# Optimization experiments

Hardware: AMD Instinct MI355X
Metric: run time of the kernel (lower is better)

The kernel has to match this reference:

```python
import jax, jax.numpy as jnp
import numpy as np

B, S, HID = 2, 2048, 2304
NH, NKV, HD = 8, 4, 256
GROUPS = NH // NKV
SCALE = 256 ** -0.5          # query_pre_attn_scalar ** -0.5
SOFTCAP = 50.0               # attn_logit_softcapping
ROPE_THETA = 10000.0


def setup_inputs() -> dict:
    key = jax.random.key(0)
    ks = jax.random.split(key, 5)
    return {
        "hidden_states": jax.random.normal(ks[0], (B, S, HID), dtype=jnp.float32),
        "wq": jax.random.normal(ks[1], (HID, NH * HD), dtype=jnp.float32) * 0.02,
        "wk": jax.random.normal(ks[2], (HID, NKV * HD), dtype=jnp.float32) * 0.02,
        "wv": jax.random.normal(ks[3], (HID, NKV * HD), dtype=jnp.float32) * 0.02,
        "wo": jax.random.normal(ks[4], (NH * HD, HID), dtype=jnp.float32) * 0.02,
    }


def _rope_cos_sin(seq_len, dim, dtype):
    inv_freq = 1.0 / (ROPE_THETA ** (jnp.arange(0, dim, 2, dtype=jnp.float32) / dim))
    pos = jnp.arange(seq_len, dtype=jnp.float32)
    freqs = pos[:, None] * inv_freq[None, :]            # [S, HD/2]
    emb = jnp.concatenate([freqs, freqs], axis=-1)      # [S, HD]
    return jnp.cos(emb).astype(dtype), jnp.sin(emb).astype(dtype)


def _rotate_half(x):
    x1, x2 = jnp.split(x, 2, axis=-1)
    return jnp.concatenate([-x2, x1], axis=-1)


def reference(hidden_states, wq, wk, wv, wo):
    b, s, _ = hidden_states.shape
    # projections -> [B, H, S, D]
    q = (hidden_states @ wq).reshape(b, s, NH, HD).transpose(0, 2, 1, 3)
    k = (hidden_states @ wk).reshape(b, s, NKV, HD).transpose(0, 2, 1, 3)
    v = (hidden_states @ wv).reshape(b, s, NKV, HD).transpose(0, 2, 1, 3)

    cos, sin = _rope_cos_sin(s, HD, q.dtype)            # [S, HD]
    q = q * cos + _rotate_half(q) * sin
    k = k * cos + _rotate_half(k) * sin

    # GQA repeat_kv
    k = jnp.repeat(k, GROUPS, axis=1)                   # [B, NH, S, D]
    v = jnp.repeat(v, GROUPS, axis=1)

    scores = jnp.einsum("bhqd,bhkd->bhqk", q, k) * SCALE
    # tanh logit softcapping
    scores = SOFTCAP * jnp.tanh(scores / SOFTCAP)
    # causal additive mask
    neg = jnp.finfo(scores.dtype).min
    causal = jnp.tril(jnp.ones((s, s), dtype=bool))
    scores = jnp.where(causal[None, None], scores, neg)

    probs = jax.nn.softmax(scores, axis=-1).astype(q.dtype)
    attn = jnp.einsum("bhqk,bhkd->bhqd", probs, v)      # [B, NH, S, D]
    attn = attn.transpose(0, 2, 1, 3).reshape(b, s, NH * HD)
    return attn @ wo
```

## Files before the change

kernel.cpp:

```cpp
#include <hip/hip_runtime.h>
#include <hip/hip_bf16.h>

typedef __attribute__((ext_vector_type(8))) short short8;
typedef __attribute__((ext_vector_type(4))) float f32x4;
typedef __attribute__((ext_vector_type(4))) unsigned short ushort4_;
typedef __attribute__((ext_vector_type(2))) unsigned long ulong2_;

__device__ __forceinline__ unsigned short f2bf(float f) {
  unsigned u = __builtin_bit_cast(unsigned, f);
  u += 0x7fff + ((u >> 16) & 1);
  return (unsigned short)(u >> 16);
}

__device__ __forceinline__ void gload16(const unsigned short* g, unsigned short* l) {
  __builtin_amdgcn_global_load_lds((const __attribute__((address_space(1))) unsigned int*)g,
                                   (__attribute__((address_space(3))) unsigned int*)l, 16, 0, 0);
}

__global__ void sincos_kernel(float2* __restrict__ table) {
  int idx = blockIdx.x * 256 + threadIdx.x;
  int s = idx >> 7, i = idx & 127;
  float inv = exp2f(-(float)i * (13.287712379549449f / 128.0f));
  float ang = (float)s * inv;
  table[idx] = make_float2(cosf(ang), sinf(ang));
}

__global__ void convert_x_kernel(const float* __restrict__ in, unsigned short* __restrict__ out, int n4) {
  int idx = blockIdx.x * 256 + threadIdx.x;
  if (idx >= n4) return;
  float4 v = ((const float4*)in)[idx];
  ushort4_ o = { f2bf(v.x), f2bf(v.y), f2bf(v.z), f2bf(v.w) };
  *(ushort4_*)(out + (size_t)idx * 4) = o;
}

__global__ __launch_bounds__(256) void wtrans_kernel(const float* __restrict__ in,
                                                     unsigned short* __restrict__ out,
                                                     int R, int C) {
  __shared__ float t[32][33];
  int tx = threadIdx.x & 31, ty = threadIdx.x >> 5;
  int r0 = blockIdx.y * 32, c0 = blockIdx.x * 32;
#pragma unroll
  for (int k = 0; k < 4; ++k) t[ty + k * 8][tx] = in[(size_t)(r0 + ty + k * 8) * C + c0 + tx];
  __syncthreads();
#pragma unroll
  for (int k = 0; k < 4; ++k) out[(size_t)(c0 + ty + k * 8) * R + r0 + tx] = f2bf(t[tx][ty + k * 8]);
}

__global__ __launch_bounds__(256) void vtrans_kernel(const float* __restrict__ qkv,
                                                     unsigned short* __restrict__ Vt) {
  __shared__ float t[32][33];
  int z = blockIdx.z; int b = z >> 2, hk = z & 3;
  const float* in = qkv + (size_t)b * 2048 * 4096 + 3072 + hk * 256;
  unsigned short* out = Vt + (size_t)z * 256 * 2048;
  int tx = threadIdx.x & 31, ty = threadIdx.x >> 5;
  int r0 = blockIdx.y * 32, c0 = blockIdx.x * 32;
#pragma unroll
  for (int k = 0; k < 4; ++k) t[ty + k * 8][tx] = in[(size_t)(r0 + ty + k * 8) * 4096 + c0 + tx];
  __syncthreads();
#pragma unroll
  for (int k = 0; k < 4; ++k) out[(size_t)(c0 + ty + k * 8) * 2048 + r0 + tx] = f2bf(t[tx][ty + k * 8]);
}

__global__ void rope_kernel(const float* __restrict__ qkv, const float2* __restrict__ table,
                            unsigned short* __restrict__ Qb, unsigned short* __restrict__ Kb) {
  int idx = blockIdx.x * 256 + threadIdx.x;
  int i = idx & 127;
  int rest = idx >> 7;
  int h12 = rest % 12;
  int rest2 = rest / 12;
  int s = rest2 & 2047;
  int b = rest2 >> 11;
  float2 cs = table[(s << 7) + i];
  size_t row = (size_t)b * 2048 + s;
  size_t col; unsigned short* out;
  if (h12 < 8) { col = (size_t)h12 * 256; out = Qb + (((size_t)(b * 8 + h12) * 2048 + s) << 8); }
  else { int hk = h12 - 8; col = 2048 + (size_t)hk * 256; out = Kb + (((size_t)(b * 4 + hk) * 2048 + s) << 8); }
  float x1 = qkv[row * 4096 + col + i];
  float x2 = qkv[row * 4096 + col + 128 + i];
  out[i]       = f2bf(x1 * cs.x - x2 * cs.y);
  out[128 + i] = f2bf(x2 * cs.x + x1 * cs.y);
}

__global__ __launch_bounds__(256) void gemm_bt_kernel(const unsigned short* __restrict__ A,
                                                      const unsigned short* __restrict__ Bt,
                                                      float* __restrict__ C, int M, int N, int K) {
  __shared__ unsigned short sA[128 * 32];
  __shared__ unsigned short sB[128 * 32];
  int tid = threadIdx.x;
  int lane = tid & 63, w = tid >> 6;
  int wr = w >> 1, wc = w & 1;
  int lr = lane & 15, lg = lane >> 4;
  long m0 = (long)blockIdx.x * 128, n0 = (long)blockIdx.y * 128;
  f32x4 acc[4][4] = {};
  int nkt = K >> 5;
  for (int kt = 0; kt < nkt; ++kt) {
    __syncthreads();
    long k0 = (long)kt * 32;
#pragma unroll
    for (int p = 0; p < 2; ++p) {
      int c = p * 256 + tid;
      int row = c >> 2, colb = (c & 3) * 8;
      gload16(&A[(m0 + row) * K + k0 + colb], &sA[c * 8]);
      gload16(&Bt[(n0 + row) * K + k0 + colb], &sB[c * 8]);
    }
    __syncthreads();
    short8 af[4], bg[4];
#pragma unroll
    for (int mi = 0; mi < 4; ++mi)
      af[mi] = *(const short8*)&sA[(wr * 64 + mi * 16 + lr) * 32 + lg * 8];
#pragma unroll
    for (int ni = 0; ni < 4; ++ni)
      bg[ni] = *(const short8*)&sB[(wc * 64 + ni * 16 + lr) * 32 + lg * 8];
#pragma unroll
    for (int mi = 0; mi < 4; ++mi)
#pragma unroll
      for (int ni = 0; ni < 4; ++ni)
        acc[mi][ni] = __builtin_amdgcn_mfma_f32_16x16x32_bf16(af[mi], bg[ni], acc[mi][ni], 0, 0, 0);
  }
#pragma unroll
  for (int mi = 0; mi < 4; ++mi)
#pragma unroll
    for (int ni = 0; ni < 4; ++ni) {
      long r = m0 + wr * 64 + mi * 16 + lg * 4;
      long cc = n0 + wc * 64 + ni * 16 + lr;
#pragma unroll
      for (int i = 0; i < 4; ++i)
        C[(r + i) * N + cc] = acc[mi][ni][i];
    }
}

__global__ __launch_bounds__(256) void attn_kernel(const unsigned short* __restrict__ Qb,
                                                   const unsigned short* __restrict__ Kb,
                                                   const unsigned short* __restrict__ Vt,
                                                   float* __restrict__ Op,
                                                   float* __restrict__ ml) {
  __shared__ unsigned short sK[64 * 256];
  __shared__ unsigned short sV[256 * 64];
  __shared__ unsigned short sP[4][16 * 64];
  int bh = blockIdx.x, y = blockIdx.y;
  int qt = 31 - (y >> 1), s = y & 1;
  int ntile = qt + 1, half = (ntile + 1) >> 1;
  int k0t = s ? half : 0, k1t = s ? ntile : half;
  int b = bh >> 3, h = bh & 7, hk = h >> 1;
  const unsigned short* Qh = Qb + ((size_t)(b * 8 + h) << 19);
  const unsigned short* Kh = Kb + ((size_t)(b * 4 + hk) << 19);
  const unsigned short* Vh = Vt + ((size_t)(b * 4 + hk) << 19);
  int tid = threadIdx.x, w = tid >> 6, lane = tid & 63;
  int lr = lane & 15, lg = lane >> 4;

  short8 qf[8];
  int qrow = qt * 64 + w * 16 + lr;
#pragma unroll
  for (int kc = 0; kc < 8; ++kc)
    qf[kc] = *(const short8*)&Qh[(size_t)qrow * 256 + kc * 32 + lg * 8];

  f32x4 acc[16] = {};
  float m_i[4], l_i[4];
#pragma unroll
  for (int i = 0; i < 4; ++i) { m_i[i] = -1e30f; l_i[i] = 0.f; }
  int qbase = qt * 64 + w * 16 + lg * 4;

  for (int kt2 = k0t; kt2 < k1t; ++kt2) {
    __syncthreads();
#pragma unroll
    for (int p = 0; p < 8; ++p) {
      int c = p * 256 + tid;
      {
        int row = c >> 5;
        int dste = (c * 8) ^ ((row & 7) << 3);
        *(ulong2_*)&sK[dste] = *(const ulong2_*)&Kh[(size_t)kt2 * 16384 + (size_t)c * 8];
      }
      {
        int r = c >> 3, ccn = c & 7;
        int dste = (r * 64 + ccn * 8) ^ ((r & 7) << 3);
        *(ulong2_*)&sV[dste] = *(const ulong2_*)&Vh[(size_t)r * 2048 + kt2 * 64 + ccn * 8];
      }
    }
    __syncthreads();

    f32x4 sf[4] = {};
#pragma unroll
    for (int nf = 0; nf < 4; ++nf) {
#pragma unroll
      for (int kc = 0; kc < 8; ++kc) {
        int row = nf * 16 + lr;
        int e = (row * 256 + kc * 32 + lg * 8) ^ ((row & 7) << 3);
        short8 kfr = *(const short8*)&sK[e];
        sf[nf] = __builtin_amdgcn_mfma_f32_16x16x32_bf16(qf[kc], kfr, sf[nf], 0, 0, 0);
      }
    }

    float pv[4][4];
    float pmax[4], psum[4];
#pragma unroll
    for (int i = 0; i < 4; ++i) pmax[i] = -1e30f;
    int kcol = kt2 * 64 + lr;
#pragma unroll
    for (int nf = 0; nf < 4; ++nf)
#pragma unroll
      for (int i = 0; i < 4; ++i) {
        float x = sf[nf][i] * (0.0625f / 50.0f);
        x = fminf(fmaxf(x, -10.f), 10.f);
        float e2 = __expf(2.f * x);
        float sc = 50.f * ((e2 - 1.f) * __builtin_amdgcn_rcpf(e2 + 1.f));
        bool masked = (kcol + nf * 16) > (qbase + i);
        sc = masked ? -1e30f : sc;
        pv[nf][i] = sc;
        pmax[i] = fmaxf(pmax[i], sc);
      }
#pragma unroll
    for (int d = 1; d < 16; d <<= 1)
#pragma unroll
      for (int i = 0; i < 4; ++i)
        pmax[i] = fmaxf(pmax[i], __shfl_xor(pmax[i], d));
    float scale_f[4];
#pragma unroll
    for (int i = 0; i < 4; ++i) {
      float m_new = fmaxf(m_i[i], pmax[i]);
      scale_f[i] = __expf(m_i[i] - m_new);
      m_i[i] = m_new;
      psum[i] = 0.f;
    }
#pragma unroll
    for (int nf = 0; nf < 4; ++nf)
#pragma unroll
      for (int i = 0; i < 4; ++i) {
        float p = __expf(pv[nf][i] - m_i[i]);
        pv[nf][i] = p;
        psum[i] += p;
      }
#pragma unroll
    for (int d = 1; d < 16; d <<= 1)
#pragma unroll
      for (int i = 0; i < 4; ++i)
        psum[i] += __shfl_xor(psum[i], d);
#pragma unroll
    for (int i = 0; i < 4; ++i)
      l_i[i] = l_i[i] * scale_f[i] + psum[i];
#pragma unroll
    for (int df = 0; df < 16; ++df)
#pragma unroll
      for (int i = 0; i < 4; ++i)
        acc[df][i] *= scale_f[i];

#pragma unroll
    for (int nf = 0; nf < 4; ++nf)
#pragma unroll
      for (int i = 0; i < 4; ++i)
        sP[w][(lg * 4 + i) * 64 + nf * 16 + lr] = f2bf(pv[nf][i]);
    asm volatile("s_waitcnt lgkmcnt(0)" ::: "memory");
    short8 pa[2];
#pragma unroll
    for (int kc2 = 0; kc2 < 2; ++kc2)
      pa[kc2] = *(const short8*)&sP[w][lr * 64 + kc2 * 32 + lg * 8];

#pragma unroll
    for (int df = 0; df < 16; ++df)
#pragma unroll
      for (int kc2 = 0; kc2 < 2; ++kc2) {
        int row = df * 16 + lr;
        int e = (row * 64 + kc2 * 32 + lg * 8) ^ ((row & 7) << 3);
        short8 vfr = *(const short8*)&sV[e];
        acc[df] = __builtin_amdgcn_mfma_f32_16x16x32_bf16(pa[kc2], vfr, acc[df], 0, 0, 0);
      }
  }

  size_t orow = (size_t)bh * 2048 + qbase;
#pragma unroll
  for (int df = 0; df < 16; ++df)
#pragma unroll
    for (int i = 0; i < 4; ++i)
      Op[(((orow + i) * 2 + s) << 8) + df * 16 + lr] = acc[df][i];
  if (lr == 0) {
#pragma unroll
    for (int i = 0; i < 4; ++i) {
      ml[(orow + i) * 4 + s * 2]     = m_i[i];
      ml[(orow + i) * 4 + s * 2 + 1] = l_i[i];
    }
  }
}

__global__ void combine_kernel(const float* __restrict__ Op, const float* __restrict__ ml,
                               unsigned short* __restrict__ attnb) {
  int idx = blockIdx.x * 256 + threadIdx.x;
  int c4 = idx & 63;
  int rest = idx >> 6;
  const float* mlp = ml + (size_t)rest * 4;
  float m0 = mlp[0], l0 = mlp[1], m1 = mlp[2], l1 = mlp[3];
  float m = fmaxf(m0, m1);
  float w0 = __expf(m0 - m), w1 = __expf(m1 - m);
  float inv = 1.0f / (l0 * w0 + l1 * w1);
  const float4 o0 = *(const float4*)&Op[(((size_t)rest * 2 + 0) << 8) + c4 * 4];
  const float4 o1 = *(const float4*)&Op[(((size_t)rest * 2 + 1) << 8) + c4 * 4];
  int row = rest & 2047, bh = rest >> 11;
  int b = bh >> 3, h = bh & 7;
  ushort4_ o;
  o.x = f2bf((o0.x * w0 + o1.x * w1) * inv);
  o.y = f2bf((o0.y * w0 + o1.y * w1) * inv);
  o.z = f2bf((o0.z * w0 + o1.z * w1) * inv);
  o.w = f2bf((o0.w * w0 + o1.w * w1) * inv);
  *(ushort4_*)&attnb[((size_t)(b * 2048 + row)) * 2048 + h * 256 + c4 * 4] = o;
}

extern "C" void kernel_launch(void* const* d_in, const int* in_sizes, int n_in,
                              void* d_out, int out_size, void* d_ws, size_t ws_size,
                              hipStream_t stream) {
  const float* hidden = (const float*)d_in[0];
  const float* wq = (const float*)d_in[1];
  const float* wk = (const float*)d_in[2];
  const float* wv = (const float*)d_in[3];
  const float* wo = (const float*)d_in[4];
  float* out = (float*)d_out;

  char* ws = (char*)d_ws;
  size_t off = 0;
  auto alloc = [&](size_t bytes) { void* p = ws + off; off += (bytes + 255) & ~255ULL; return p; };
  float2* table = (float2*)alloc((size_t)2048 * 128 * sizeof(float2));
  unsigned short* Xb    = (unsigned short*)alloc((size_t)4096 * 2304 * 2);
  unsigned short* WallT = (unsigned short*)alloc((size_t)4096 * 2304 * 2);
  unsigned short* WoT   = (unsigned short*)alloc((size_t)2304 * 2048 * 2);
  float*          QKV   = (float*)alloc((size_t)4096 * 4096 * 4);
  unsigned short* Qb    = (unsigned short*)alloc((size_t)2 * 8 * 2048 * 256 * 2);
  unsigned short* Kb    = (unsigned short*)alloc((size_t)2 * 4 * 2048 * 256 * 2);
  unsigned short* Vt    = (unsigned short*)alloc((size_t)2 * 4 * 2048 * 256 * 2);
  float*          Op    = QKV;
  float*          mlbuf = (float*)table;
  unsigned short* attnb = Xb;

  sincos_kernel<<<1024, 256, 0, stream>>>(table);
  convert_x_kernel<<<9216, 256, 0, stream>>>(hidden, Xb, 2359296);
  wtrans_kernel<<<dim3(64, 72), 256, 0, stream>>>(wq, WallT, 2304, 2048);
  wtrans_kernel<<<dim3(32, 72), 256, 0, stream>>>(wk, WallT + (size_t)2048 * 2304, 2304, 1024);
  wtrans_kernel<<<dim3(32, 72), 256, 0, stream>>>(wv, WallT + (size_t)3072 * 2304, 2304, 1024);
  wtrans_kernel<<<dim3(72, 64), 256, 0, stream>>>(wo, WoT, 2048, 2304);
  gemm_bt_kernel<<<dim3(32, 32), 256, 0, stream>>>(Xb, WallT, QKV, 4096, 4096, 2304);
  rope_kernel<<<24576, 256, 0, stream>>>(QKV, table, Qb, Kb);
  vtrans_kernel<<<dim3(8, 64, 8), 256, 0, stream>>>(QKV, Vt);
  attn_kernel<<<dim3(16, 64), 256, 0, stream>>>(Qb, Kb, Vt, Op, mlbuf);
  combine_kernel<<<8192, 256, 0, stream>>>(Op, mlbuf, attnb);
  gemm_bt_kernel<<<dim3(32, 18), 256, 0, stream>>>(attnb, WoT, out, 4096, 2304, 2048);
}
```

Before: 470.2 us.

## Use fixed softcap max in softmax, double-buffer K asynchronously, read V from global

Because softcapping bounds every logit to at most 50, the attention kernel drops the online running max and rescaling. It computes probabilities directly as exp(-100/(e^{2z}+1)), which is exp(score-50), and the combine kernel simply sums the partial outputs and normalizers. K tiles are now double-buffered in LDS and prefetched with asynchronous global-to-LDS loads, while V fragments are read straight from global memory instead of being staged in LDS. This removes shuffle reductions, extra exponentials and accumulator rescaling. The costs are less coalesced V loads and a risk of underflow if all logits in a row are near -50.

```diff
diff --git a/kernel.cpp b/kernel.cpp
--- a/kernel.cpp
+++ b/kernel.cpp
@@ -134,8 +134,7 @@
                                                    const unsigned short* __restrict__ Vt,
                                                    float* __restrict__ Op,
                                                    float* __restrict__ ml) {
-  __shared__ unsigned short sK[64 * 256];
-  __shared__ unsigned short sV[256 * 64];
+  __shared__ unsigned short sK[2][64 * 256];
   __shared__ unsigned short sP[4][16 * 64];
   int bh = blockIdx.x, y = blockIdx.y;
   int qt = 31 - (y >> 1), s = y & 1;
@@ -155,28 +154,30 @@
     qf[kc] = *(const short8*)&Qh[(size_t)qrow * 256 + kc * 32 + lg * 8];
 
   f32x4 acc[16] = {};
-  float m_i[4], l_i[4];
-#pragma unroll
-  for (int i = 0; i < 4; ++i) { m_i[i] = -1e30f; l_i[i] = 0.f; }
+  float l_i[4] = {0.f, 0.f, 0.f, 0.f};
   int qbase = qt * 64 + w * 16 + lg * 4;
 
-  for (int kt2 = k0t; kt2 < k1t; ++kt2) {
-    __syncthreads();
-#pragma unroll
-    for (int p = 0; p < 8; ++p) {
-      int c = p * 256 + tid;
-      {
-        int row = c >> 5;
-        int dste = (c * 8) ^ ((row & 7) << 3);
-        *(ulong2_*)&sK[dste] = *(const ulong2_*)&Kh[(size_t)kt2 * 16384 + (size_t)c * 8];
+  int nt = k1t - k0t;
+#pragma unroll
+  for (int p = 0; p < 8; ++p) {
+    int c = p * 256 + tid;
+    int src = c ^ ((c >> 5) & 7);
+    gload16(&Kh[(size_t)k0t * 16384 + (size_t)src * 8], &sK[0][c * 8]);
+  }
+  __syncthreads();
+
+  for (int it = 0; it < nt; ++it) {
+    int kt2 = k0t + it;
+    const unsigned short* sKc = sK[it & 1];
+    if (it + 1 < nt) {
+      unsigned short* sKn = sK[(it + 1) & 1];
+#pragma unroll
+      for (int p = 0; p < 8; ++p) {
+        int c = p * 256 + tid;
+        int src = c ^ ((c >> 5) & 7);
+        gload16(&Kh[(size_t)(kt2 + 1) * 16384 + (size_t)src * 8], &sKn[c * 8]);
       }
-      {
-        int r = c >> 3, ccn = c & 7;
-        int dste = (r * 64 + ccn * 8) ^ ((r & 7) << 3);
-        *(ulong2_*)&sV[dste] = *(const ulong2_*)&Vh[(size_t)r * 2048 + kt2 * 64 + ccn * 8];
-      }
-    }
-    __syncthreads();
+    }
 
     f32x4 sf[4] = {};
 #pragma unroll
@@ -185,48 +186,24 @@
       for (int kc = 0; kc < 8; ++kc) {
         int row = nf * 16 + lr;
         int e = (row * 256 + kc * 32 + lg * 8) ^ ((row & 7) << 3);
-        short8 kfr = *(const short8*)&sK[e];
+        short8 kfr = *(const short8*)&sKc[e];
         sf[nf] = __builtin_amdgcn_mfma_f32_16x16x32_bf16(qf[kc], kfr, sf[nf], 0, 0, 0);
       }
     }
 
-    float pv[4][4];
-    float pmax[4], psum[4];
-#pragma unroll
-    for (int i = 0; i < 4; ++i) pmax[i] = -1e30f;
+    float psum[4] = {0.f, 0.f, 0.f, 0.f};
     int kcol = kt2 * 64 + lr;
 #pragma unroll
     for (int nf = 0; nf < 4; ++nf)
 #pragma unroll
       for (int i = 0; i < 4; ++i) {
-        float x = sf[nf][i] * (0.0625f / 50.0f);
-        x = fminf(fmaxf(x, -10.f), 10.f);
-        float e2 = __expf(2.f * x);
-        float sc = 50.f * ((e2 - 1.f) * __builtin_amdgcn_rcpf(e2 + 1.f));
+        float z2 = sf[nf][i] * 0.0025f;
+        z2 = fminf(fmaxf(z2, -20.f), 20.f);
+        float e2 = __expf(z2);
+        float p = __expf(-100.f * __builtin_amdgcn_rcpf(e2 + 1.f));
         bool masked = (kcol + nf * 16) > (qbase + i);
-        sc = masked ? -1e30f : sc;
-        pv[nf][i] = sc;
-        pmax[i] = fmaxf(pmax[i], sc);
-      }
-#pragma unroll
-    for (int d = 1; d < 16; d <<= 1)
-#pragma unroll
-      for (int i = 0; i < 4; ++i)
-        pmax[i] = fmaxf(pmax[i], __shfl_xor(pmax[i], d));
-    float scale_f[4];
-#pragma unroll
-    for (int i = 0; i < 4; ++i) {
-      float m_new = fmaxf(m_i[i], pmax[i]);
-      scale_f[i] = __expf(m_i[i] - m_new);
-      m_i[i] = m_new;
-      psum[i] = 0.f;
-    }
-#pragma unroll
-    for (int nf = 0; nf < 4; ++nf)
-#pragma unroll
-      for (int i = 0; i < 4; ++i) {
-        float p = __expf(pv[nf][i] - m_i[i]);
-        pv[nf][i] = p;
+        p = masked ? 0.f : p;
+        sf[nf][i] = p;
         psum[i] += p;
       }
 #pragma unroll
@@ -235,19 +212,13 @@
       for (int i = 0; i < 4; ++i)
         psum[i] += __shfl_xor(psum[i], d);
 #pragma unroll
-    for (int i = 0; i < 4; ++i)
-      l_i[i] = l_i[i] * scale_f[i] + psum[i];
-#pragma unroll
-    for (int df = 0; df < 16; ++df)
+    for (int i = 0; i < 4; ++i) l_i[i] += psum[i];
+
+#pragma unroll
+    for (int nf = 0; nf < 4; ++nf)
 #pragma unroll
       for (int i = 0; i < 4; ++i)
-        acc[df][i] *= scale_f[i];
-
-#pragma unroll
-    for (int nf = 0; nf < 4; ++nf)
-#pragma unroll
-      for (int i = 0; i < 4; ++i)
-        sP[w][(lg * 4 + i) * 64 + nf * 16 + lr] = f2bf(pv[nf][i]);
+        sP[w][(lg * 4 + i) * 64 + nf * 16 + lr] = f2bf(sf[nf][i]);
     asm volatile("s_waitcnt lgkmcnt(0)" ::: "memory");
     short8 pa[2];
 #pragma unroll
@@ -255,14 +226,14 @@
       pa[kc2] = *(const short8*)&sP[w][lr * 64 + kc2 * 32 + lg * 8];
 
 #pragma unroll
-    for (int df = 0; df < 16; ++df)
+    for (int df = 0; df < 16; ++df) {
 #pragma unroll
       for (int kc2 = 0; kc2 < 2; ++kc2) {
-        int row = df * 16 + lr;
-        int e = (row * 64 + kc2 * 32 + lg * 8) ^ ((row & 7) << 3);
-        short8 vfr = *(const short8*)&sV[e];
+        short8 vfr = *(const short8*)&Vh[(size_t)(df * 16 + lr) * 2048 + kt2 * 64 + kc2 * 32 + lg * 8];
         acc[df] = __builtin_amdgcn_mfma_f32_16x16x32_bf16(pa[kc2], vfr, acc[df], 0, 0, 0);
       }
+    }
+    __syncthreads();
   }
 
   size_t orow = (size_t)bh * 2048 + qbase;
@@ -273,10 +244,8 @@
       Op[(((orow + i) * 2 + s) << 8) + df * 16 + lr] = acc[df][i];
   if (lr == 0) {
 #pragma unroll
-    for (int i = 0; i < 4; ++i) {
-      ml[(orow + i) * 4 + s * 2]     = m_i[i];
-      ml[(orow + i) * 4 + s * 2 + 1] = l_i[i];
-    }
+    for (int i = 0; i < 4; ++i)
+      ml[(orow + i) * 2 + s] = l_i[i];
   }
 }
 
@@ -285,20 +254,17 @@
   int idx = blockIdx.x * 256 + threadIdx.x;
   int c4 = idx & 63;
   int rest = idx >> 6;
-  const float* mlp = ml + (size_t)rest * 4;
-  float m0 = mlp[0], l0 = mlp[1], m1 = mlp[2], l1 = mlp[3];
-  float m = fmaxf(m0, m1);
-  float w0 = __expf(m0 - m), w1 = __expf(m1 - m);
-  float inv = 1.0f / (l0 * w0 + l1 * w1);
+  float l0 = ml[(size_t)rest * 2], l1 = ml[(size_t)rest * 2 + 1];
+  float inv = 1.0f / (l0 + l1);
   const float4 o0 = *(const float4*)&Op[(((size_t)rest * 2 + 0) << 8) + c4 * 4];
   const float4 o1 = *(const float4*)&Op[(((size_t)rest * 2 + 1) << 8) + c4 * 4];
   int row = rest & 2047, bh = rest >> 11;
   int b = bh >> 3, h = bh & 7;
   ushort4_ o;
-  o.x = f2bf((o0.x * w0 + o1.x * w1) * inv);
-  o.y = f2bf((o0.y * w0 + o1.y * w1) * inv);
-  o.z = f2bf((o0.z * w0 + o1.z * w1) * inv);
-  o.w = f2bf((o0.w * w0 + o1.w * w1) * inv);
+  o.x = f2bf((o0.x + o1.x) * inv);
+  o.y = f2bf((o0.y + o1.y) * inv);
+  o.z = f2bf((o0.z + o1.z) * inv);
+  o.w = f2bf((o0.w + o1.w) * inv);
   *(ushort4_*)&attnb[((size_t)(b * 2048 + row)) * 2048 + h * 256 + c4 * 4] = o;
 }
 
```

Result: slower. 554.0 us (+17.8%).
